# Performance work log

Measured on AMD Instinct MI355X. Metric: run time of the kernel, lower is better.

The kernel has to match this reference:

```python
import math
import jax, jax.numpy as jnp
import numpy as np

D_MODEL = 1024
N_HEADS = 16
D_K = D_MODEL // N_HEADS
B = 8
L = 1024
LATTICE = (4, 4)
TWO_PI = 2.0 * math.pi


def _build_neighbors():
    """Replicates LatticeMultiHeadAttention._build_neighbors (Moore 8-neighborhood)."""
    positions = [divmod(i, LATTICE[1]) for i in range(N_HEADS)]
    idx = np.full((N_HEADS, 8), -1, dtype=np.int64)
    w = np.zeros((N_HEADS, 8), dtype=np.float32)
    for i, (r1, c1) in enumerate(positions):
        k = 0
        for dr in (-1, 0, 1):
            for dc in (-1, 0, 1):
                if dr == 0 and dc == 0:
                    continue
                if k >= 8:
                    break
                r2, c2 = r1 + dr, c1 + dc
                for j, (r, c) in enumerate(positions):
                    if (r, c) == (r2, c2):
                        idx[i, k] = j
                        w[i, k] = math.exp(-math.hypot(dr, dc))
                        k += 1
                        break
    return idx, w


def setup_inputs() -> dict:
    key = jax.random.key(0)
    ks = jax.random.split(key, 8)
    s = 1.0 / math.sqrt(D_MODEL)
    nbr_idx_np, nbr_w_np = _build_neighbors()
    return {
        "query": jax.random.normal(ks[0], (B, L, D_MODEL), jnp.float32),
        "key_": jax.random.normal(ks[1], (B, L, D_MODEL), jnp.float32),
        "value": jax.random.normal(ks[2], (B, L, D_MODEL), jnp.float32),
        # head-stacked projection weights, stored as [H, d_model, d_k] (x @ W)
        "Wq": jax.random.normal(ks[3], (N_HEADS, D_MODEL, D_K), jnp.float32) * s,
        "Wk": jax.random.normal(ks[4], (N_HEADS, D_MODEL, D_K), jnp.float32) * s,
        "Wv": jax.random.normal(ks[5], (N_HEADS, D_MODEL, D_K), jnp.float32) * s,
        "Wo": jax.random.normal(ks[6], (D_MODEL, D_MODEL), jnp.float32) * s,
        "bo": jax.random.normal(ks[7], (D_MODEL,), jnp.float32) * 0.01,
        # buffers: initial phases (0.0), intrinsic freqs 1 + 0.1*h, lattice tables
        "phases0": jnp.zeros((N_HEADS,), jnp.float32),
        "freqs": jnp.asarray(1.0 + 0.1 * np.arange(N_HEADS), jnp.float32),
        "nbr_w": jnp.asarray(nbr_w_np),
        "nbr_idx": jnp.asarray(nbr_idx_np),
    }


def _updated_phases(phases0, freqs, nbr_w, nbr_idx):
    # multi-head batched Kuramoto step (note: coupling_strength is NOT used here,
    # matching the original forward), then the per-head internal step (empty
    # neighbor_phases branch adds another 0.01 * intrinsic_freq).
    valid = (nbr_idx >= 0).astype(phases0.dtype)        # [H,8]
    nbr_ph = phases0[jnp.clip(nbr_idx, 0, None)] * valid  # [H,8]
    phase_diff = nbr_ph - phases0[:, None]
    force = (nbr_w * jnp.sin(phase_diff)).sum(axis=1)     # [H]
    p1 = jnp.mod(phases0 + 0.01 * (freqs + force), TWO_PI)
    p2 = jnp.mod(p1 + 0.01 * freqs, TWO_PI)
    return p2


def reference(query, key_, value, Wq, Wk, Wv, Wo, bo, phases0, freqs, nbr_w, nbr_idx):
    # phases are torch buffers updated under no_grad -> constants w.r.t. autodiff
    p2 = jax.lax.stop_gradient(
        _updated_phases(phases0, freqs, nbr_w, nbr_idx))
    bias = 0.1 * jnp.cos(p2)                               # [H]

    Q = jnp.einsum('bld,hdk->bhlk', query, Wq)
    K = jnp.einsum('bld,hdk->bhlk', key_, Wk)
    V = jnp.einsum('bld,hdk->bhlk', value, Wv)

    scores = jnp.einsum('bhlk,bhmk->bhlm', Q, K) / jnp.sqrt(
        jnp.asarray(D_K, Q.dtype))
    scores = scores + bias[None, :, None, None]
    attn = jax.nn.softmax(scores, axis=-1)                 # [B,H,L,L]
    ctx = jnp.einsum('bhlm,bhmk->bhlk', attn, V)           # [B,H,L,d_k]
    ctx = ctx.transpose(0, 2, 1, 3).reshape(query.shape[0], query.shape[1], D_MODEL)
    return ctx @ Wo + bo                                   # out_proj
```

## Files before the change

kernel.cpp:

```cpp
#include <hip/hip_runtime.h>
#include <hip/hip_bf16.h>
#include <stdint.h>


typedef unsigned short u16;
typedef __bf16 bf16_t;
typedef bf16_t bf16x8 __attribute__((ext_vector_type(8)));
typedef float f32x4 __attribute__((ext_vector_type(4)));

#define DEVI static __device__ __forceinline__
#define MFMA16(a, b, c) __builtin_amdgcn_mfma_f32_16x16x32_bf16((a), (b), (c), 0, 0, 0)

DEVI void gload_lds16(const void* g, void* l) {
  __builtin_amdgcn_global_load_lds((__attribute__((address_space(1))) void*)g,
                                   (__attribute__((address_space(3))) void*)l, 16, 0, 0);
}

DEVI u16 f2bf(float x) {
  bf16_t b = (bf16_t)x;
  u16 u;
  __builtin_memcpy(&u, &b, 2);
  return u;
}

__global__ __launch_bounds__(256) void prep(const float* __restrict__ Wq,
                                            const float* __restrict__ Wk,
                                            const float* __restrict__ Wv,
                                            const float* __restrict__ Wo,
                                            const float* __restrict__ q,
                                            const float* __restrict__ k,
                                            const float* __restrict__ v,
                                            u16* __restrict__ ws) {
  int bx = blockIdx.x;
  if (bx < 2048) {
    int id = bx * 256 + threadIdx.x;
    int mat = id >> 17;
    int rem = id & 131071;
    const float* src = (mat == 0) ? Wq : (mat == 1) ? Wk : (mat == 2) ? Wv : Wo;
    u16* dst = ws + (size_t)mat * 1048576;
    if (mat < 3) {
      int jb = rem & 7;
      int kk = (rem >> 3) & 1023;
      int h = rem >> 13;
      const float* s = src + h * 65536 + kk * 64 + jb * 8;
      float4 a = *(const float4*)s;
      float4 b = *(const float4*)(s + 4);
      float vv[8] = {a.x, a.y, a.z, a.w, b.x, b.y, b.z, b.w};
#pragma unroll
      for (int jj = 0; jj < 8; jj++)
        dst[(size_t)(h * 64 + jb * 8 + jj) * 1024 + kk] = f2bf(vv[jj]);
    } else {
      int cb = rem & 127;
      int d = rem >> 7;
      const float* s = src + d * 1024 + cb * 8;
      float4 a = *(const float4*)s;
      float4 b = *(const float4*)(s + 4);
      float vv[8] = {a.x, a.y, a.z, a.w, b.x, b.y, b.z, b.w};
#pragma unroll
      for (int jj = 0; jj < 8; jj++)
        dst[(size_t)(cb * 8 + jj) * 1024 + d] = f2bf(vv[jj]);
    }
  } else {
    int id = (bx - 2048) * 256 + threadIdx.x;
    int t = id >> 21;
    size_t rem = (size_t)(id & 2097151) * 4;
    const float* src = (t == 0) ? q : (t == 1) ? k : v;
    float4 a = *(const float4*)(src + rem);
    ushort4 st;
    st.x = f2bf(a.x); st.y = f2bf(a.y); st.z = f2bf(a.z); st.w = f2bf(a.w);
    *(ushort4*)(ws + 4194304 + (size_t)t * 8388608 + rem) = st;
  }
}

__global__ __launch_bounds__(256) void gemm_qkv(const u16* __restrict__ WT,
                                                const u16* __restrict__ X,
                                                u16* __restrict__ Qw,
                                                u16* __restrict__ Kw,
                                                u16* __restrict__ Vw) {
  __shared__ __align__(16) u16 sA[128 * 32];
  __shared__ __align__(16) u16 sB[128 * 32];
  int id = blockIdx.x + 8 * (blockIdx.y + 64 * blockIdx.z);
  int xcd = id & 7, j = id >> 3;
  int mtile = j & 7;
  int g = xcd * 24 + (j >> 3);
  int z = g >> 6;
  int nt = g & 63;
  const u16* A = WT + (size_t)z * 1048576;
  const u16* Bx = X + (size_t)z * 8388608;
  u16* out = (z == 0) ? Qw : (z == 1) ? Kw : Vw;
  float oscale = (z == 0) ? 0.125f : 1.0f;

  int tid = threadIdx.x;
  int wid = tid >> 6, lane = tid & 63, quad = lane >> 4, l16 = lane & 15;
  int wm = wid >> 1, wn = wid & 1;
  int m0 = mtile * 128, n0 = nt * 128;

  f32x4 acc[4][4];
#pragma unroll
  for (int i = 0; i < 4; i++)
#pragma unroll
    for (int jj = 0; jj < 4; jj++) acc[i][jj] = {0.f, 0.f, 0.f, 0.f};

  for (int k0 = 0; k0 < 1024; k0 += 32) {
#pragma unroll
    for (int p = 0; p < 2; p++) {
      int cl = p * 256 + tid;
      int r = cl >> 2, kc = cl & 3;
      gload_lds16(A + (size_t)(m0 + r) * 1024 + k0 + kc * 8,
                  (char*)sA + (p * 256 + wid * 64) * 16);
      gload_lds16(Bx + (size_t)(n0 + r) * 1024 + k0 + kc * 8,
                  (char*)sB + (p * 256 + wid * 64) * 16);
    }
    __syncthreads();
    bf16x8 af[4], bfr[4];
#pragma unroll
    for (int mt = 0; mt < 4; mt++)
      af[mt] = *(const bf16x8*)((const char*)sA + ((wm * 64 + mt * 16 + l16) * 64 + quad * 16));
#pragma unroll
    for (int ntf = 0; ntf < 4; ntf++)
      bfr[ntf] = *(const bf16x8*)((const char*)sB + ((wn * 64 + ntf * 16 + l16) * 64 + quad * 16));
#pragma unroll
    for (int mt = 0; mt < 4; mt++)
#pragma unroll
      for (int ntf = 0; ntf < 4; ntf++) acc[mt][ntf] = MFMA16(af[mt], bfr[ntf], acc[mt][ntf]);
    __syncthreads();
  }

#pragma unroll
  for (int mt = 0; mt < 4; mt++) {
    int m = m0 + wm * 64 + mt * 16 + quad * 4;
#pragma unroll
    for (int ntf = 0; ntf < 4; ntf++) {
      int n = n0 + wn * 64 + ntf * 16 + l16;
      f32x4 v = acc[mt][ntf];
      int b = n >> 10, l = n & 1023, h = m >> 6, dk = m & 63;
      if (z < 2) {
        ushort4 st;
        st.x = f2bf(v[0] * oscale); st.y = f2bf(v[1] * oscale);
        st.z = f2bf(v[2] * oscale); st.w = f2bf(v[3] * oscale);
        *(ushort4*)(out + ((size_t)((b * 16 + h) * 1024 + l) * 64 + dk)) = st;
      } else {
        size_t base = ((size_t)((b * 16 + h) * 64 + dk)) * 1024 + l;
        out[base] = f2bf(v[0]);
        out[base + 1024] = f2bf(v[1]);
        out[base + 2048] = f2bf(v[2]);
        out[base + 3072] = f2bf(v[3]);
      }
    }
  }
}

__global__ __launch_bounds__(256) void gemm_out(const u16* __restrict__ A,
                                                const u16* __restrict__ Bx,
                                                float* __restrict__ outf,
                                                const float* __restrict__ bias) {
  __shared__ __align__(16) u16 sA[128 * 32];
  __shared__ __align__(16) u16 sB[128 * 32];
  int id = blockIdx.x + 8 * blockIdx.y;
  int xcd = id & 7, j = id >> 3;
  int mtile = j & 7;
  int nt = xcd * 8 + (j >> 3);
  int tid = threadIdx.x;
  int wid = tid >> 6, lane = tid & 63, quad = lane >> 4, l16 = lane & 15;
  int wm = wid >> 1, wn = wid & 1;
  int m0 = mtile * 128, n0 = nt * 128;

  f32x4 acc[4][4];
#pragma unroll
  for (int i = 0; i < 4; i++)
#pragma unroll
    for (int jj = 0; jj < 4; jj++) acc[i][jj] = {0.f, 0.f, 0.f, 0.f};

  for (int k0 = 0; k0 < 1024; k0 += 32) {
#pragma unroll
    for (int p = 0; p < 2; p++) {
      int cl = p * 256 + tid;
      int r = cl >> 2, kc = cl & 3;
      gload_lds16(A + (size_t)(m0 + r) * 1024 + k0 + kc * 8,
                  (char*)sA + (p * 256 + wid * 64) * 16);
      gload_lds16(Bx + (size_t)(n0 + r) * 1024 + k0 + kc * 8,
                  (char*)sB + (p * 256 + wid * 64) * 16);
    }
    __syncthreads();
    bf16x8 af[4], bfr[4];
#pragma unroll
    for (int mt = 0; mt < 4; mt++)
      af[mt] = *(const bf16x8*)((const char*)sA + ((wm * 64 + mt * 16 + l16) * 64 + quad * 16));
#pragma unroll
    for (int ntf = 0; ntf < 4; ntf++)
      bfr[ntf] = *(const bf16x8*)((const char*)sB + ((wn * 64 + ntf * 16 + l16) * 64 + quad * 16));
#pragma unroll
    for (int mt = 0; mt < 4; mt++)
#pragma unroll
      for (int ntf = 0; ntf < 4; ntf++) acc[mt][ntf] = MFMA16(af[mt], bfr[ntf], acc[mt][ntf]);
    __syncthreads();
  }

#pragma unroll
  for (int mt = 0; mt < 4; mt++) {
    int m = m0 + wm * 64 + mt * 16 + quad * 4;
#pragma unroll
    for (int ntf = 0; ntf < 4; ntf++) {
      int n = n0 + wn * 64 + ntf * 16 + l16;
      f32x4 v = acc[mt][ntf];
      float4 st;
      st.x = v[0] + bias[m];
      st.y = v[1] + bias[m + 1];
      st.z = v[2] + bias[m + 2];
      st.w = v[3] + bias[m + 3];
      *(float4*)(outf + ((size_t)n * 1024 + m)) = st;
    }
  }
}

__global__ __launch_bounds__(256, 4) void attn_k(const u16* __restrict__ Q,
                                                 const u16* __restrict__ K,
                                                 const u16* __restrict__ VT,
                                                 u16* __restrict__ CTX) {
  __shared__ __align__(16) u16 sQ[128 * 64];
  __shared__ __align__(16) u16 sK[64 * 64];
  __shared__ __align__(16) u16 sV[64 * 64];
  int tid = threadIdx.x;
  int wid = tid >> 6, lane = tid & 63, quad = lane >> 4, l16 = lane & 15;
  int id = blockIdx.x + 8 * blockIdx.y;
  int xcd = id & 7, j = id >> 3;
  int qt = j & 7;
  int bh = xcd * 16 + (j >> 3);
  const u16* Qb = Q + (size_t)bh * 65536;
  const u16* Kb = K + (size_t)bh * 65536;
  const u16* Vb = VT + (size_t)bh * 65536;
  int q0 = qt * 128;

#pragma unroll
  for (int p = 0; p < 4; p++) {
    int cl = p * 256 + tid;
    int r = cl >> 3, c = cl & 7, g = c ^ (r & 7);
    gload_lds16(Qb + (size_t)(q0 + r) * 64 + g * 8, (char*)sQ + (p * 256 + wid * 64) * 16);
  }
  __syncthreads();

  bf16x8 bq[2][2];
#pragma unroll
  for (int qf = 0; qf < 2; qf++) {
    int row = wid * 32 + qf * 16 + l16;
#pragma unroll
    for (int ks = 0; ks < 2; ks++) {
      int ch = (ks * 4 + quad) ^ (row & 7);
      bq[qf][ks] = *(const bf16x8*)((const char*)sQ + row * 128 + ch * 16);
    }
  }

  u16* sPw = sQ + wid * 2048;

  f32x4 oacc[4][2];
#pragma unroll
  for (int i = 0; i < 4; i++) {
    oacc[i][0] = {0.f, 0.f, 0.f, 0.f};
    oacc[i][1] = {0.f, 0.f, 0.f, 0.f};
  }
  float lsum[2] = {0.f, 0.f};

  for (int lk0 = 0; lk0 < 1024; lk0 += 64) {
#pragma unroll
    for (int p = 0; p < 2; p++) {
      int cl = p * 256 + tid;
      int r = cl >> 3, c = cl & 7, g = c ^ (r & 7);
      gload_lds16(Kb + (size_t)(lk0 + r) * 64 + g * 8, (char*)sK + (p * 256 + wid * 64) * 16);
      gload_lds16(Vb + (size_t)r * 1024 + lk0 + g * 8, (char*)sV + (p * 256 + wid * 64) * 16);
    }
    __syncthreads();

    f32x4 s[4][2];
#pragma unroll
    for (int mt = 0; mt < 4; mt++) {
      s[mt][0] = {0.f, 0.f, 0.f, 0.f};
      s[mt][1] = {0.f, 0.f, 0.f, 0.f};
    }
#pragma unroll
    for (int ks = 0; ks < 2; ks++) {
#pragma unroll
      for (int mt = 0; mt < 4; mt++) {
        int row = mt * 16 + l16;
        int ch = (ks * 4 + quad) ^ (row & 7);
        bf16x8 a = *(const bf16x8*)((const char*)sK + row * 128 + ch * 16);
        s[mt][0] = MFMA16(a, bq[0][ks], s[mt][0]);
        s[mt][1] = MFMA16(a, bq[1][ks], s[mt][1]);
      }
    }

#pragma unroll
    for (int qf = 0; qf < 2; qf++) {
      int row = qf * 16 + l16;
#pragma unroll
      for (int mt = 0; mt < 4; mt++) {
        float p0 = __expf(s[mt][qf][0]);
        float p1 = __expf(s[mt][qf][1]);
        float p2 = __expf(s[mt][qf][2]);
        float p3 = __expf(s[mt][qf][3]);
        lsum[qf] += (p0 + p1) + (p2 + p3);
        ushort4 st;
        st.x = f2bf(p0); st.y = f2bf(p1); st.z = f2bf(p2); st.w = f2bf(p3);
        int ch = (2 * mt + (quad >> 1)) ^ (row & 7);
        *(ushort4*)((char*)sPw + row * 128 + ch * 16 + (quad & 1) * 8) = st;
      }
    }
    asm volatile("s_waitcnt lgkmcnt(0)" ::: "memory");

    bf16x8 bp[2][2];
#pragma unroll
    for (int qf = 0; qf < 2; qf++) {
      int row = qf * 16 + l16;
#pragma unroll
      for (int c = 0; c < 2; c++) {
        int ch = (c * 4 + quad) ^ (row & 7);
        bp[qf][c] = *(const bf16x8*)((const char*)sPw + row * 128 + ch * 16);
      }
    }
#pragma unroll
    for (int c = 0; c < 2; c++) {
#pragma unroll
      for (int mt = 0; mt < 4; mt++) {
        int row = mt * 16 + l16;
        int ch = (c * 4 + quad) ^ (row & 7);
        bf16x8 a = *(const bf16x8*)((const char*)sV + row * 128 + ch * 16);
        oacc[mt][0] = MFMA16(a, bp[0][c], oacc[mt][0]);
        oacc[mt][1] = MFMA16(a, bp[1][c], oacc[mt][1]);
      }
    }
    __syncthreads();
  }

#pragma unroll
  for (int qf = 0; qf < 2; qf++) {
    lsum[qf] += __shfl_xor(lsum[qf], 16, 64);
    lsum[qf] += __shfl_xor(lsum[qf], 32, 64);
  }
  float inv0 = 1.f / lsum[0], inv1 = 1.f / lsum[1];

  int b = bh >> 4, h = bh & 15;
#pragma unroll
  for (int qf = 0; qf < 2; qf++) {
    int qg = q0 + wid * 32 + qf * 16 + l16;
    float inv = qf ? inv1 : inv0;
#pragma unroll
    for (int mt = 0; mt < 4; mt++) {
      int dk = mt * 16 + quad * 4;
      ushort4 st;
      st.x = f2bf(oacc[mt][qf][0] * inv);
      st.y = f2bf(oacc[mt][qf][1] * inv);
      st.z = f2bf(oacc[mt][qf][2] * inv);
      st.w = f2bf(oacc[mt][qf][3] * inv);
      *(ushort4*)(CTX + (((size_t)(b * 1024 + qg) * 16 + h) * 64 + dk)) = st;
    }
  }
}

extern "C" void kernel_launch(void* const* d_in, const int* in_sizes, int n_in,
                              void* d_out, int out_size, void* d_ws, size_t ws_size,
                              hipStream_t stream) {
  (void)in_sizes; (void)n_in; (void)out_size;
  const float* query = (const float*)d_in[0];
  const float* key_ = (const float*)d_in[1];
  const float* value = (const float*)d_in[2];
  const float* Wq = (const float*)d_in[3];
  const float* Wk = (const float*)d_in[4];
  const float* Wv = (const float*)d_in[5];
  const float* Wo = (const float*)d_in[6];
  const float* bo = (const float*)d_in[7];

  u16* ws = (u16*)d_ws;
  u16* WT = ws;
  u16* X = ws + 4194304;
  u16* Qw = ws + 29360128;
  u16* Kw = ws + 37748736;
  u16* Vw = ws + 46137344;
  u16* Cw = X;
  float* outp = (float*)d_out;

  prep<<<26624, 256, 0, stream>>>(Wq, Wk, Wv, Wo, query, key_, value, ws);
  gemm_qkv<<<dim3(8, 64, 3), 256, 0, stream>>>(WT, X, Qw, Kw, Vw);
  attn_k<<<dim3(8, 128), 256, 0, stream>>>(Qw, Kw, Vw, Cw);
  gemm_out<<<dim3(8, 64), 256, 0, stream>>>(WT + 3145728, Cw, outp, bo);
}
```

Measured before the change: 306.7 us.

## Rewrite QKV GEMM as 256x256 tile, double-buffered, swizzled-LDS pipelined kernel

The QKV projection GEMM moves from a 128x128 tile with 4 waves and a single-buffered K=32 loop to a 256x256 tile with 8 waves and double-buffered K=64 stages. Global-to-LDS loads are interleaved with MFMA phases using barriers, s_setprio and partial vmcnt waits, and LDS rows are XOR-swizzled to avoid bank conflicts. The aim is to hide memory latency and raise arithmetic intensity. In exchange it uses 128KB of LDS per block, needs more registers, and launches only 384 blocks, which may limit occupancy.

```diff
diff --git a/kernel.cpp b/kernel.cpp
--- a/kernel.cpp
+++ b/kernel.cpp
@@ -72,75 +72,161 @@
   }
 }
 
-__global__ __launch_bounds__(256) void gemm_qkv(const u16* __restrict__ WT,
-                                                const u16* __restrict__ X,
-                                                u16* __restrict__ Qw,
-                                                u16* __restrict__ Kw,
-                                                u16* __restrict__ Vw) {
-  __shared__ __align__(16) u16 sA[128 * 32];
-  __shared__ __align__(16) u16 sB[128 * 32];
-  int id = blockIdx.x + 8 * (blockIdx.y + 64 * blockIdx.z);
-  int xcd = id & 7, j = id >> 3;
-  int mtile = j & 7;
-  int g = xcd * 24 + (j >> 3);
-  int z = g >> 6;
-  int nt = g & 63;
-  const u16* A = WT + (size_t)z * 1048576;
-  const u16* Bx = X + (size_t)z * 8388608;
+__global__ __launch_bounds__(512, 2) void gemm_qkv(const u16* __restrict__ WT,
+                                                   const u16* __restrict__ X,
+                                                   u16* __restrict__ Qw,
+                                                   u16* __restrict__ Kw,
+                                                   u16* __restrict__ Vw) {
+  __shared__ __align__(1024) u16 lds[65536];
+  int tid = threadIdx.x;
+  int wid = tid >> 6, lane = tid & 63, quad = lane >> 4, l16 = lane & 15;
+  int wm = wid >> 2, wn = wid & 3;
+
+  int orig = blockIdx.x;
+  int wgid = (orig & 7) * 48 + (orig >> 3);
+  int z = wgid >> 7;
+  int rr = wgid & 127;
+  int nt0 = rr >> 2, mt0 = rr & 3;
+  const u16* Ag = WT + (size_t)z * 1048576;
+  const u16* Bg = X + (size_t)z * 8388608;
   u16* out = (z == 0) ? Qw : (z == 1) ? Kw : Vw;
   float oscale = (z == 0) ? 0.125f : 1.0f;
-
-  int tid = threadIdx.x;
-  int wid = tid >> 6, lane = tid & 63, quad = lane >> 4, l16 = lane & 15;
-  int wm = wid >> 1, wn = wid & 1;
-  int m0 = mtile * 128, n0 = nt * 128;
-
-  f32x4 acc[4][4];
-#pragma unroll
-  for (int i = 0; i < 4; i++)
-#pragma unroll
-    for (int jj = 0; jj < 4; jj++) acc[i][jj] = {0.f, 0.f, 0.f, 0.f};
-
-  for (int k0 = 0; k0 < 1024; k0 += 32) {
-#pragma unroll
-    for (int p = 0; p < 2; p++) {
-      int cl = p * 256 + tid;
-      int r = cl >> 2, kc = cl & 3;
-      gload_lds16(A + (size_t)(m0 + r) * 1024 + k0 + kc * 8,
-                  (char*)sA + (p * 256 + wid * 64) * 16);
-      gload_lds16(Bx + (size_t)(n0 + r) * 1024 + k0 + kc * 8,
-                  (char*)sB + (p * 256 + wid * 64) * 16);
-    }
-    __syncthreads();
-    bf16x8 af[4], bfr[4];
-#pragma unroll
-    for (int mt = 0; mt < 4; mt++)
-      af[mt] = *(const bf16x8*)((const char*)sA + ((wm * 64 + mt * 16 + l16) * 64 + quad * 16));
-#pragma unroll
-    for (int ntf = 0; ntf < 4; ntf++)
-      bfr[ntf] = *(const bf16x8*)((const char*)sB + ((wn * 64 + ntf * 16 + l16) * 64 + quad * 16));
-#pragma unroll
-    for (int mt = 0; mt < 4; mt++)
-#pragma unroll
-      for (int ntf = 0; ntf < 4; ntf++) acc[mt][ntf] = MFMA16(af[mt], bfr[ntf], acc[mt][ntf]);
-    __syncthreads();
-  }
-
-#pragma unroll
-  for (int mt = 0; mt < 4; mt++) {
-    int m = m0 + wm * 64 + mt * 16 + quad * 4;
-#pragma unroll
-    for (int ntf = 0; ntf < 4; ntf++) {
-      int n = n0 + wn * 64 + ntf * 16 + l16;
-      f32x4 v = acc[mt][ntf];
-      int b = n >> 10, l = n & 1023, h = m >> 6, dk = m & 63;
+  int m0 = mt0 << 8, n0 = nt0 << 8;
+
+  const u16* gA = Ag + (size_t)m0 * 1024;
+  const u16* gB = Bg + (size_t)n0 * 1024;
+  int rA = tid >> 3;
+  int lc = (tid & 7) ^ (rA & 7);
+  size_t goff = (size_t)rA * 1024 + lc * 8;
+
+  char* ldsc = (char*)lds;
+  int rx = l16 & 7;
+  int baA = wm * 16384;
+  int baB = (2 + (wn >> 1)) * 16384 + (wn & 1) * 8192;
+
+  auto stageA = [&](int buf, int half, int kt) {
+    const u16* g = gA + (size_t)(half * 128) * 1024 + kt * 64 + goff;
+    char* d = ldsc + (buf * 4 + half) * 16384 + wid * 1024;
+    gload_lds16(g, d);
+    gload_lds16(g + 65536, d + 8192);
+  };
+  auto stageB = [&](int buf, int half, int kt) {
+    const u16* g = gB + (size_t)(half * 128) * 1024 + kt * 64 + goff;
+    char* d = ldsc + (buf * 4 + 2 + half) * 16384 + wid * 1024;
+    gload_lds16(g, d);
+    gload_lds16(g + 65536, d + 8192);
+  };
+  auto rdA = [&](int buf, int mh, int mf, int ks) -> bf16x8 {
+    return *(const bf16x8*)(ldsc + (buf << 16) + baA + (mh * 64 + mf * 16 + l16) * 128 +
+                            ((((ks << 2) | quad) ^ rx) << 4));
+  };
+  auto rdB = [&](int buf, int nf, int ks) -> bf16x8 {
+    return *(const bf16x8*)(ldsc + (buf << 16) + baB + (nf * 16 + l16) * 128 +
+                            ((((ks << 2) | quad) ^ rx) << 4));
+  };
+
+  f32x4 acc[8][4];
+#pragma unroll
+  for (int i = 0; i < 8; ++i)
+#pragma unroll
+    for (int j = 0; j < 4; ++j) acc[i][j] = {0.f, 0.f, 0.f, 0.f};
+  bf16x8 af[4][2], bfr[4][2];
+
+  stageA(0, 0, 0); stageA(0, 1, 0);
+  stageB(0, 0, 0); stageB(0, 1, 0);
+  stageB(1, 0, 1); stageB(1, 1, 1);
+  asm volatile("s_waitcnt vmcnt(4)" ::: "memory");
+  __builtin_amdgcn_s_barrier();
+
+  for (int t = 0; t < 16; ++t) {
+    int cur = t & 1, nxt = cur ^ 1;
+
+#pragma unroll
+    for (int mf = 0; mf < 4; ++mf)
+#pragma unroll
+      for (int ks = 0; ks < 2; ++ks) af[mf][ks] = rdA(cur, 0, mf, ks);
+#pragma unroll
+    for (int nf = 0; nf < 2; ++nf)
+#pragma unroll
+      for (int ks = 0; ks < 2; ++ks) bfr[nf][ks] = rdB(cur, nf, ks);
+    if (t < 15) stageA(nxt, 0, t + 1);
+    __builtin_amdgcn_s_barrier();
+    __builtin_amdgcn_s_setprio(1);
+#pragma unroll
+    for (int ks = 0; ks < 2; ++ks)
+#pragma unroll
+      for (int mf = 0; mf < 4; ++mf)
+#pragma unroll
+        for (int nf = 0; nf < 2; ++nf)
+          acc[mf][nf] = MFMA16(af[mf][ks], bfr[nf][ks], acc[mf][nf]);
+    __builtin_amdgcn_s_setprio(0);
+    __builtin_amdgcn_s_barrier();
+
+#pragma unroll
+    for (int nf = 2; nf < 4; ++nf)
+#pragma unroll
+      for (int ks = 0; ks < 2; ++ks) bfr[nf][ks] = rdB(cur, nf, ks);
+    if (t < 15) stageA(nxt, 1, t + 1);
+    __builtin_amdgcn_s_barrier();
+    __builtin_amdgcn_s_setprio(1);
+#pragma unroll
+    for (int ks = 0; ks < 2; ++ks)
+#pragma unroll
+      for (int mf = 0; mf < 4; ++mf)
+#pragma unroll
+        for (int nf = 2; nf < 4; ++nf)
+          acc[mf][nf] = MFMA16(af[mf][ks], bfr[nf][ks], acc[mf][nf]);
+    __builtin_amdgcn_s_setprio(0);
+    __builtin_amdgcn_s_barrier();
+
+#pragma unroll
+    for (int mf = 0; mf < 4; ++mf)
+#pragma unroll
+      for (int ks = 0; ks < 2; ++ks) af[mf][ks] = rdA(cur, 1, mf, ks);
+    if (t < 14) stageB(cur, 0, t + 2);
+    __builtin_amdgcn_s_barrier();
+    __builtin_amdgcn_s_setprio(1);
+#pragma unroll
+    for (int ks = 0; ks < 2; ++ks)
+#pragma unroll
+      for (int mf = 0; mf < 4; ++mf)
+#pragma unroll
+        for (int nf = 2; nf < 4; ++nf)
+          acc[4 + mf][nf] = MFMA16(af[mf][ks], bfr[nf][ks], acc[4 + mf][nf]);
+    __builtin_amdgcn_s_setprio(0);
+    __builtin_amdgcn_s_barrier();
+
+    if (t < 14) stageB(cur, 1, t + 2);
+    __builtin_amdgcn_s_barrier();
+    __builtin_amdgcn_s_setprio(1);
+#pragma unroll
+    for (int ks = 0; ks < 2; ++ks)
+#pragma unroll
+      for (int mf = 0; mf < 4; ++mf)
+#pragma unroll
+        for (int nf = 0; nf < 2; ++nf)
+          acc[4 + mf][nf] = MFMA16(af[mf][ks], bfr[nf][ks], acc[4 + mf][nf]);
+    __builtin_amdgcn_s_setprio(0);
+    asm volatile("s_waitcnt vmcnt(4)" ::: "memory");
+    __builtin_amdgcn_s_barrier();
+  }
+
+#pragma unroll
+  for (int mfg = 0; mfg < 8; ++mfg) {
+    int m = m0 + wm * 128 + mfg * 16 + quad * 4;
+    int h = m >> 6, dk = m & 63;
+#pragma unroll
+    for (int nf = 0; nf < 4; ++nf) {
+      int n = n0 + wn * 64 + nf * 16 + l16;
+      int bb = n >> 10, l = n & 1023;
+      f32x4 v = acc[mfg][nf];
       if (z < 2) {
         ushort4 st;
         st.x = f2bf(v[0] * oscale); st.y = f2bf(v[1] * oscale);
         st.z = f2bf(v[2] * oscale); st.w = f2bf(v[3] * oscale);
-        *(ushort4*)(out + ((size_t)((b * 16 + h) * 1024 + l) * 64 + dk)) = st;
+        *(ushort4*)(out + ((size_t)((bb * 16 + h) * 1024 + l) * 64 + dk)) = st;
       } else {
-        size_t base = ((size_t)((b * 16 + h) * 64 + dk)) * 1024 + l;
+        size_t base = ((size_t)((bb * 16 + h) * 64 + dk)) * 1024 + l;
         out[base] = f2bf(v[0]);
         out[base + 1024] = f2bf(v[1]);
         out[base + 2048] = f2bf(v[2]);
@@ -378,7 +464,7 @@
   float* outp = (float*)d_out;
 
   prep<<<26624, 256, 0, stream>>>(Wq, Wk, Wv, Wo, query, key_, value, ws);
-  gemm_qkv<<<dim3(8, 64, 3), 256, 0, stream>>>(WT, X, Qw, Kw, Vw);
+  gemm_qkv<<<dim3(384), 512, 0, stream>>>(WT, X, Qw, Kw, Vw);
   attn_k<<<dim3(8, 128), 256, 0, stream>>>(Qw, Kw, Vw, Cw);
   gemm_out<<<dim3(8, 64), 256, 0, stream>>>(WT + 3145728, Cw, outp, bo);
 }
```

Result: no change. 309.6 us (+0.9%).
